# Performance work log

Measured on AMD Instinct MI355X. Metric: run time of the kernel, lower is better.

Reference implementation:

```python
import jax, jax.numpy as jnp
import numpy as np

INPUT_DIM = 256
EMBED_DIM = 256
NUM_HEADS = 8
HEAD_DIM = EMBED_DIM // NUM_HEADS
N_TOKENS = 11136
N_BATCH = 16


def _xavier(key, shape):
    fan_out, fan_in = shape
    bound = np.sqrt(6.0 / (fan_in + fan_out)).astype(np.float32)
    return jax.random.uniform(key, shape, jnp.float32, -bound, bound)


def setup_inputs() -> dict:
    key = jax.random.key(0)
    k_x, k_ids, k_qkv, k_o = jax.random.split(key, 4)
    x = jax.random.normal(k_x, (N_TOKENS, INPUT_DIM), jnp.float32)
    batch_ids = jnp.sort(jax.random.randint(k_ids, (N_TOKENS,), 0, N_BATCH)).astype(jnp.int32)
    qkv_w = _xavier(k_qkv, (3 * EMBED_DIM, INPUT_DIM))
    qkv_b = jnp.zeros((3 * EMBED_DIM,), jnp.float32)
    o_w = _xavier(k_o, (EMBED_DIM, EMBED_DIM))
    o_b = jnp.zeros((EMBED_DIM,), jnp.float32)
    return {"x": x, "batch_ids": batch_ids, "qkv_w": qkv_w, "qkv_b": qkv_b,
            "o_w": o_w, "o_b": o_b}


def reference(x, batch_ids, qkv_w, qkv_b, o_w, o_b):
    # batch_ids is concrete metadata (mirrors np.unique on CPU in the original).
    ids = np.asarray(batch_ids)
    vals, counts = np.unique(ids, return_counts=True)
    B = len(vals)
    S = int(counts.max())
    offsets = np.concatenate([np.zeros(1, np.int64), np.cumsum(counts)[:-1]])
    seg = np.searchsorted(vals, ids)               # segment index per token
    pos = np.arange(ids.shape[0]) - offsets[seg]   # position within segment

    qkv = x @ qkv_w.T + qkv_b                      # [N, 3E]
    # pad_sequence with padding_value=1 -> scatter tokens into an all-ones buffer
    fin = jnp.ones((B, S, 3 * EMBED_DIM), qkv.dtype).at[seg, pos].set(qkv)
    # padded rows sum to exactly 3E (all ones) -> mask True marks padding
    pad_mask = fin.sum(-1) >= fin.shape[-1]        # [B, S]

    qkv4 = fin.reshape(B, S, NUM_HEADS, 3 * HEAD_DIM).transpose(0, 2, 1, 3)
    q, k, v = jnp.split(qkv4, 3, axis=-1)          # each [B, H, S, hd]

    logits = jnp.einsum('bhqd,bhkd->bhqk', q, k) * (HEAD_DIM ** -0.5)
    logits = jnp.where(pad_mask[:, None, None, :], -jnp.inf, logits)
    attn = jax.nn.softmax(logits, axis=-1)         # [B, H, S, S]

    out = jnp.einsum('bhqk,bhkd->bhqd', attn, v)
    out = out.transpose(0, 2, 1, 3).reshape(B, S, EMBED_DIM)
    out = out[seg, pos]                            # unpad -> [N, E]
    return out @ o_w.T + o_b
```

## Files before the change

kernel.cpp:

```cpp
#include <hip/hip_runtime.h>
#include <stdint.h>


#define N_TOK 11136
#define E 256
#define H 8
#define HD 32

typedef __attribute__((ext_vector_type(8))) __bf16 bf16x8;
typedef __attribute__((ext_vector_type(8))) unsigned short u16x8;
typedef __attribute__((ext_vector_type(4))) float f32x4;

__device__ __forceinline__ unsigned short f2bf(float f) {
  unsigned int u = __float_as_uint(f);
  u = (u + 0x7FFFu + ((u >> 16) & 1u)) >> 16;
  return (unsigned short)u;
}
__device__ __forceinline__ float bf2f(unsigned short s) {
  return __uint_as_float(((unsigned int)s) << 16);
}
__device__ __forceinline__ bf16x8 ld8(const unsigned short* p) {
  return *(const bf16x8*)p;
}

__global__ void k_split(const float* __restrict__ x, const float* __restrict__ qw,
                        const float* __restrict__ ow, const int* __restrict__ ids,
                        unsigned short* __restrict__ xhi, unsigned short* __restrict__ xlo,
                        unsigned short* __restrict__ whi, unsigned short* __restrict__ wlo,
                        unsigned short* __restrict__ owb, int* __restrict__ offs) {
  if (blockIdx.x == 0 && threadIdx.x < 17) {
    int b = threadIdx.x, lo = 0, hi = N_TOK;
    while (lo < hi) { int mid = (lo + hi) >> 1; if (ids[mid] < b) lo = mid + 1; else hi = mid; }
    offs[b] = lo;
  }
  const int NX4 = N_TOK * E / 4;
  const int NW4 = 3 * E * E / 4;
  const int NO4 = E * E / 4;
  int total = NX4 + NW4 + NO4;
  for (int i = blockIdx.x * blockDim.x + threadIdx.x; i < total;
       i += gridDim.x * blockDim.x) {
    if (i < NX4) {
      float4 v = ((const float4*)x)[i];
      ushort4 hv, lv;
      hv.x = f2bf(v.x); lv.x = f2bf(v.x - bf2f(hv.x));
      hv.y = f2bf(v.y); lv.y = f2bf(v.y - bf2f(hv.y));
      hv.z = f2bf(v.z); lv.z = f2bf(v.z - bf2f(hv.z));
      hv.w = f2bf(v.w); lv.w = f2bf(v.w - bf2f(hv.w));
      ((ushort4*)xhi)[i] = hv; ((ushort4*)xlo)[i] = lv;
    } else if (i < NX4 + NW4) {
      int j = i - NX4;
      float4 v = ((const float4*)qw)[j];
      ushort4 hv, lv;
      hv.x = f2bf(v.x); lv.x = f2bf(v.x - bf2f(hv.x));
      hv.y = f2bf(v.y); lv.y = f2bf(v.y - bf2f(hv.y));
      hv.z = f2bf(v.z); lv.z = f2bf(v.z - bf2f(hv.z));
      hv.w = f2bf(v.w); lv.w = f2bf(v.w - bf2f(hv.w));
      ((ushort4*)whi)[j] = hv; ((ushort4*)wlo)[j] = lv;
    } else {
      int j = i - NX4 - NW4;
      float4 v = ((const float4*)ow)[j];
      ushort4 hv;
      hv.x = f2bf(v.x); hv.y = f2bf(v.y); hv.z = f2bf(v.z); hv.w = f2bf(v.w);
      ((ushort4*)owb)[j] = hv;
    }
  }
}

#define QK_BSTRIDE 264
#define QSCALE (0.17677669529663687f * 1.4426950408889634f)
__global__ __launch_bounds__(256, 3) void k_qkv(
    const unsigned short* __restrict__ xhi, const unsigned short* __restrict__ xlo,
    const unsigned short* __restrict__ whi, const unsigned short* __restrict__ wlo,
    const float* __restrict__ qkv_b,
    unsigned short* __restrict__ Qb, unsigned short* __restrict__ Kb,
    unsigned short* __restrict__ Vt) {
  int bid = blockIdx.x + 16 * blockIdx.y;
  int xcd = bid & 7;
  int j8 = bid >> 3;
  int colb = j8 & 15;
  int tile = (j8 >> 4) * 8 + xcd;
  if (tile >= 58) return;
  int col0 = colb * 48;
  __shared__ __align__(16) unsigned short Bhi[48 * QK_BSTRIDE];
  __shared__ __align__(16) unsigned short Blo[48 * QK_BSTRIDE];
  int tid = threadIdx.x;
  int w = tid >> 6, lane = tid & 63, m = lane & 15, quad = lane >> 4;
  int rowb = tile * 192 + w * 48;

  {
    const u16x8* wh8 = (const u16x8*)(whi + (size_t)col0 * E);
    const u16x8* wl8 = (const u16x8*)(wlo + (size_t)col0 * E);
#pragma unroll
    for (int i = 0; i < 6; ++i) {
      int flat = i * 256 + tid;
      int row = flat >> 5, c8 = flat & 31;
      *(u16x8*)(Bhi + row * QK_BSTRIDE + c8 * 8) = wh8[flat];
      *(u16x8*)(Blo + row * QK_BSTRIDE + c8 * 8) = wl8[flat];
    }
  }
  __syncthreads();

  f32x4 acc[3][3] = {};
  bf16x8 ahn[3], aln[3];
#pragma unroll
  for (int mt = 0; mt < 3; ++mt) {
    const size_t ro = (size_t)(rowb + mt * 16 + m) * E + quad * 8;
    ahn[mt] = ld8(xhi + ro);
    aln[mt] = ld8(xlo + ro);
  }
  for (int kc = 0; kc < 8; ++kc) {
    bf16x8 ah[3], al[3];
#pragma unroll
    for (int mt = 0; mt < 3; ++mt) { ah[mt] = ahn[mt]; al[mt] = aln[mt]; }
    int kon = (kc < 7 ? kc + 1 : kc) * 32 + quad * 8;
#pragma unroll
    for (int mt = 0; mt < 3; ++mt) {
      const size_t ro = (size_t)(rowb + mt * 16 + m) * E + kon;
      ahn[mt] = ld8(xhi + ro);
      aln[mt] = ld8(xlo + ro);
    }
    int ko = kc * 32 + quad * 8;
#pragma unroll
    for (int t = 0; t < 3; ++t) {
      bf16x8 bh = ld8(Bhi + (16 * t + m) * QK_BSTRIDE + ko);
      bf16x8 bl = ld8(Blo + (16 * t + m) * QK_BSTRIDE + ko);
#pragma unroll
      for (int mt = 0; mt < 3; ++mt) {
        acc[mt][t] = __builtin_amdgcn_mfma_f32_16x16x32_bf16(ah[mt], bh, acc[mt][t], 0, 0, 0);
        acc[mt][t] = __builtin_amdgcn_mfma_f32_16x16x32_bf16(ah[mt], bl, acc[mt][t], 0, 0, 0);
        acc[mt][t] = __builtin_amdgcn_mfma_f32_16x16x32_bf16(al[mt], bh, acc[mt][t], 0, 0, 0);
      }
    }
  }
#pragma unroll
  for (int t = 0; t < 3; ++t) {
    int j = col0 + 16 * t + m;
    int hd = j / 96;
    int rr = j - hd * 96;
    float bias = qkv_b[j];
#pragma unroll
    for (int mt = 0; mt < 3; ++mt) {
      int tokb = rowb + mt * 16 + quad * 4;
      if (rr < 64) {
        float qsc = (rr < 32) ? QSCALE : 1.0f;
        unsigned short* dst = (rr < 32) ? (Qb + (size_t)hd * N_TOK * HD + rr)
                                        : (Kb + (size_t)hd * N_TOK * HD + (rr - 32));
#pragma unroll
        for (int r = 0; r < 4; ++r)
          dst[(size_t)(tokb + r) * HD] = f2bf((acc[mt][t][r] + bias) * qsc);
      } else {
        int d = rr - 64;
        ushort4 pk;
        pk.x = f2bf(acc[mt][t][0] + bias); pk.y = f2bf(acc[mt][t][1] + bias);
        pk.z = f2bf(acc[mt][t][2] + bias); pk.w = f2bf(acc[mt][t][3] + bias);
        *(ushort4*)(Vt + (size_t)(hd * HD + d) * N_TOK + tokb) = pk;
      }
    }
  }
}

#define PSTRIDE 72
#define VSTR 72
__global__ __launch_bounds__(256, 4) void k_attn(
    const int* __restrict__ ids, const int* __restrict__ offs,
    const unsigned short* __restrict__ Qb, const unsigned short* __restrict__ Kb,
    const unsigned short* __restrict__ Vt,
    unsigned short* __restrict__ attnb) {
  __shared__ __align__(16) unsigned short Kl[2][64 * 32];
  __shared__ __align__(16) unsigned short Vl[2][32 * VSTR];
  __shared__ __align__(16) unsigned short ldsP[4][16 * PSTRIDE];
  __shared__ int bred[8];
  int tid = threadIdx.x;
  int w = tid >> 6, lane = tid & 63;
  int m = lane & 15, quad = lane >> 4;
  int h = blockIdx.x;
  int tok0 = blockIdx.y * 64;
  int q0 = tok0 + w * 16;
  unsigned short* P = ldsP[w];
  int tok = q0 + m;
  int b = ids[tok];
  int st = offs[b], en = offs[b + 1];
  int kmin = st, kmax = en, stM = st, enm = en;
#pragma unroll
  for (int d = 1; d <= 8; d <<= 1) {
    kmin = min(kmin, __shfl_xor(kmin, d));
    kmax = max(kmax, __shfl_xor(kmax, d));
    stM  = max(stM,  __shfl_xor(stM,  d));
    enm  = min(enm,  __shfl_xor(enm,  d));
  }
  if (lane == 0) { bred[w] = kmin; bred[4 + w] = kmax; }
  __syncthreads();
  int kminB = min(min(bred[0], bred[1]), min(bred[2], bred[3]));
  int kmaxB = max(max(bred[4], bred[5]), max(bred[6], bred[7]));
  int k0beg = kminB & ~63;

  const unsigned short* Kbase = Kb + (size_t)h * N_TOK * HD;
  const unsigned short* Vbase = Vt + (size_t)h * HD * N_TOK;
  bf16x8 qf = ld8(Qb + (size_t)(h * N_TOK + tok) * HD + quad * 8);

  int krow = w * 16 + (lane >> 2);
  int kgof = (lane & 3) * 8;
  int vrow = w * 8 + (lane >> 3);
  int vgof = (lane & 7) * 8;

  bf16x8 kg = ld8(Kbase + (size_t)(k0beg + krow) * HD + kgof);
  bf16x8 vg = ld8(Vbase + (size_t)vrow * N_TOK + k0beg + vgof);
  *(bf16x8*)(&Kl[0][krow * 32 + kgof]) = kg;
  *(bf16x8*)(&Vl[0][vrow * VSTR + vgof]) = vg;
  __syncthreads();

  float lsum = 0.f;
  f32x4 o0 = {}, o1 = {};
  int buf = 0;
  for (int k0 = k0beg; k0 < kmaxB; k0 += 64) {
    int k1 = (k0 + 64 < kmaxB) ? (k0 + 64) : k0;
    kg = ld8(Kbase + (size_t)(k1 + krow) * HD + kgof);
    vg = ld8(Vbase + (size_t)vrow * N_TOK + k1 + vgof);
    const unsigned short* Kc = &Kl[buf][0];
    const unsigned short* Vc = &Vl[buf][0];
    f32x4 s[4];
#pragma unroll
    for (int i = 0; i < 4; ++i) {
      bf16x8 kf = ld8(Kc + (16 * i + m) * 32 + quad * 8);
      f32x4 z = {};
      s[i] = __builtin_amdgcn_mfma_f32_16x16x32_bf16(kf, qf, z, 0, 0, 0);
    }
    bool interior = (k0 >= stM && k0 + 64 <= enm);
    int jb = k0 + quad * 4;
#pragma unroll
    for (int i = 0; i < 4; ++i) {
      float p[4];
#pragma unroll
      for (int r = 0; r < 4; ++r) {
        float sv = s[i][r];
        if (!interior) {
          int j = jb + 16 * i + r;
          sv = (j >= st && j < en) ? sv : -3e38f;
        }
        float e;
        asm("v_exp_f32 %0, %1" : "=v"(e) : "v"(sv));
        p[r] = e;
      }
      lsum += (p[0] + p[1]) + (p[2] + p[3]);
      unsigned int b0 = __float_as_uint(p[0]) + 0x8000u;
      unsigned int b1 = __float_as_uint(p[1]) + 0x8000u;
      unsigned int b2 = __float_as_uint(p[2]) + 0x8000u;
      unsigned int b3 = __float_as_uint(p[3]) + 0x8000u;
      uint2 pk;
      pk.x = (b1 & 0xFFFF0000u) | (b0 >> 16);
      pk.y = (b3 & 0xFFFF0000u) | (b2 >> 16);
      *(uint2*)(P + m * PSTRIDE + 16 * i + quad * 4) = pk;
    }
#pragma unroll
    for (int c = 0; c < 2; ++c) {
      bf16x8 pf  = ld8(P + m * PSTRIDE + 32 * c + quad * 8);
      bf16x8 vf0 = ld8(Vc + m * VSTR + 32 * c + quad * 8);
      bf16x8 vf1 = ld8(Vc + (16 + m) * VSTR + 32 * c + quad * 8);
      o0 = __builtin_amdgcn_mfma_f32_16x16x32_bf16(vf0, pf, o0, 0, 0, 0);
      o1 = __builtin_amdgcn_mfma_f32_16x16x32_bf16(vf1, pf, o1, 0, 0, 0);
    }
    *(bf16x8*)(&Kl[buf ^ 1][krow * 32 + kgof]) = kg;
    *(bf16x8*)(&Vl[buf ^ 1][vrow * VSTR + vgof]) = vg;
    __syncthreads();
    buf ^= 1;
  }
  lsum += __shfl_xor(lsum, 16);
  lsum += __shfl_xor(lsum, 32);
  float inv = 1.0f / lsum;
  ushort4 pk0, pk1;
  pk0.x = f2bf(o0[0] * inv); pk0.y = f2bf(o0[1] * inv);
  pk0.z = f2bf(o0[2] * inv); pk0.w = f2bf(o0[3] * inv);
  pk1.x = f2bf(o1[0] * inv); pk1.y = f2bf(o1[1] * inv);
  pk1.z = f2bf(o1[2] * inv); pk1.w = f2bf(o1[3] * inv);
  *(ushort4*)(attnb + (size_t)tok * E + h * HD + quad * 4) = pk0;
  *(ushort4*)(attnb + (size_t)tok * E + h * HD + 16 + quad * 4) = pk1;
}

__global__ __launch_bounds__(256, 4) void k_oproj(
    const unsigned short* __restrict__ attnb, const unsigned short* __restrict__ owb,
    const float* __restrict__ ob, float* __restrict__ out) {
  __shared__ __align__(16) unsigned short Bo[64 * QK_BSTRIDE];
  int tid = threadIdx.x;
  int w = tid >> 6, lane = tid & 63, m = lane & 15, quad = lane >> 4;
  int tok0 = blockIdx.x * 64, col0 = blockIdx.y * 64;
  {
    const u16x8* o8 = (const u16x8*)(owb + (size_t)col0 * E);
#pragma unroll
    for (int i = 0; i < 8; ++i) {
      int flat = i * 256 + tid;
      int row = flat >> 5, c8 = flat & 31;
      *(u16x8*)(Bo + row * QK_BSTRIDE + c8 * 8) = o8[flat];
    }
  }
  __syncthreads();
  f32x4 acc[4] = {};
  int arow = tok0 + 16 * w + m;
  const unsigned short* abase = attnb + (size_t)arow * E + quad * 8;
  bf16x8 an = ld8(abase);
  for (int kc = 0; kc < 8; ++kc) {
    bf16x8 a = an;
    an = ld8(abase + (kc < 7 ? kc + 1 : kc) * 32);
    int ko = kc * 32 + quad * 8;
#pragma unroll
    for (int t = 0; t < 4; ++t) {
      bf16x8 b = ld8(Bo + (16 * t + m) * QK_BSTRIDE + ko);
      acc[t] = __builtin_amdgcn_mfma_f32_16x16x32_bf16(a, b, acc[t], 0, 0, 0);
    }
  }
#pragma unroll
  for (int t = 0; t < 4; ++t) {
    int j = col0 + 16 * t + m;
    float bias = ob[j];
#pragma unroll
    for (int r = 0; r < 4; ++r) {
      int tok = tok0 + 16 * w + quad * 4 + r;
      out[(size_t)tok * E + j] = acc[t][r] + bias;
    }
  }
}

extern "C" void kernel_launch(void* const* d_in, const int* in_sizes, int n_in,
                              void* d_out, int out_size, void* d_ws, size_t ws_size,
                              hipStream_t stream) {
  const float* x   = (const float*)d_in[0];
  const int*   ids = (const int*)d_in[1];
  const float* qw  = (const float*)d_in[2];
  const float* qb  = (const float*)d_in[3];
  const float* ow  = (const float*)d_in[4];
  const float* ob  = (const float*)d_in[5];
  float* out = (float*)d_out;

  char* p = (char*)d_ws;
  auto alloc = [&](size_t bytes) {
    char* r = p;
    p += (bytes + 255) & ~(size_t)255;
    return r;
  };
  int* offs = (int*)alloc(32 * sizeof(int));
  unsigned short* xhi = (unsigned short*)alloc((size_t)N_TOK * E * 2);
  unsigned short* xlo = (unsigned short*)alloc((size_t)N_TOK * E * 2);
  unsigned short* whi = (unsigned short*)alloc((size_t)3 * E * E * 2);
  unsigned short* wlo = (unsigned short*)alloc((size_t)3 * E * E * 2);
  unsigned short* owb = (unsigned short*)alloc((size_t)E * E * 2);
  unsigned short* Qb  = (unsigned short*)alloc((size_t)N_TOK * E * 2);
  unsigned short* Kb  = (unsigned short*)alloc((size_t)N_TOK * E * 2);
  unsigned short* Vt  = (unsigned short*)alloc((size_t)N_TOK * E * 2);
  unsigned short* att = (unsigned short*)alloc((size_t)N_TOK * E * 2);

  k_split<<<dim3(1712), dim3(256), 0, stream>>>(x, qw, ow, ids, xhi, xlo, whi, wlo, owb, offs);
  k_qkv<<<dim3(16, 64), dim3(256), 0, stream>>>(xhi, xlo, whi, wlo, qb, Qb, Kb, Vt);
  k_attn<<<dim3(H, N_TOK / 64), dim3(256), 0, stream>>>(ids, offs, Qb, Kb, Vt, att);
  k_oproj<<<dim3(N_TOK / 64, E / 64), dim3(256), 0, stream>>>(att, owb, ob, out);
}
```

Measured before the change: 154.7 us.

## Process two query tiles per warp in attention to reuse K/V tiles

Each attention block now handles 128 query tokens instead of 64, with every wave computing two 16-row query tiles against the same K/V tile held in LDS. This halves the K/V global loads and LDS staging per query and doubles MFMA work per barrier, aiming to cut memory and synchronisation overhead. In exchange, register pressure and LDS use grow, the grid halves (8x87 blocks), and the key range per block widens, which may add masked work when a block straddles segment boundaries.

Measured after the change: 164.6 us. +6.4%, slower.

```diff
diff --git a/kernel.cpp b/kernel.cpp
--- a/kernel.cpp
+++ b/kernel.cpp
@@ -168,27 +168,29 @@
     unsigned short* __restrict__ attnb) {
   __shared__ __align__(16) unsigned short Kl[2][64 * 32];
   __shared__ __align__(16) unsigned short Vl[2][32 * VSTR];
-  __shared__ __align__(16) unsigned short ldsP[4][16 * PSTRIDE];
+  __shared__ __align__(16) unsigned short ldsP[8][16 * PSTRIDE];
   __shared__ int bred[8];
   int tid = threadIdx.x;
   int w = tid >> 6, lane = tid & 63;
   int m = lane & 15, quad = lane >> 4;
   int h = blockIdx.x;
-  int tok0 = blockIdx.y * 64;
-  int q0 = tok0 + w * 16;
-  unsigned short* P = ldsP[w];
-  int tok = q0 + m;
-  int b = ids[tok];
-  int st = offs[b], en = offs[b + 1];
-  int kmin = st, kmax = en, stM = st, enm = en;
+  int q0 = blockIdx.y * 128 + w * 16;
+  int tok0 = q0 + m, tok1 = q0 + 64 + m;
+  int b0 = ids[tok0], b1 = ids[tok1];
+  int st0 = offs[b0], en0 = offs[b0 + 1];
+  int st1 = offs[b1], en1 = offs[b1 + 1];
+  int kminW = min(st0, st1), kmaxW = max(en0, en1);
+  int stM0 = st0, enm0 = en0, stM1 = st1, enm1 = en1;
 #pragma unroll
   for (int d = 1; d <= 8; d <<= 1) {
-    kmin = min(kmin, __shfl_xor(kmin, d));
-    kmax = max(kmax, __shfl_xor(kmax, d));
-    stM  = max(stM,  __shfl_xor(stM,  d));
-    enm  = min(enm,  __shfl_xor(enm,  d));
-  }
-  if (lane == 0) { bred[w] = kmin; bred[4 + w] = kmax; }
+    kminW = min(kminW, __shfl_xor(kminW, d));
+    kmaxW = max(kmaxW, __shfl_xor(kmaxW, d));
+    stM0 = max(stM0, __shfl_xor(stM0, d));
+    enm0 = min(enm0, __shfl_xor(enm0, d));
+    stM1 = max(stM1, __shfl_xor(stM1, d));
+    enm1 = min(enm1, __shfl_xor(enm1, d));
+  }
+  if (lane == 0) { bred[w] = kminW; bred[4 + w] = kmaxW; }
   __syncthreads();
   int kminB = min(min(bred[0], bred[1]), min(bred[2], bred[3]));
   int kmaxB = max(max(bred[4], bred[5]), max(bred[6], bred[7]));
@@ -196,7 +198,10 @@
 
   const unsigned short* Kbase = Kb + (size_t)h * N_TOK * HD;
   const unsigned short* Vbase = Vt + (size_t)h * HD * N_TOK;
-  bf16x8 qf = ld8(Qb + (size_t)(h * N_TOK + tok) * HD + quad * 8);
+  bf16x8 qf0 = ld8(Qb + (size_t)(h * N_TOK + tok0) * HD + quad * 8);
+  bf16x8 qf1 = ld8(Qb + (size_t)(h * N_TOK + tok1) * HD + quad * 8);
+  unsigned short* P0 = ldsP[2 * w];
+  unsigned short* P1 = ldsP[2 * w + 1];
 
   int krow = w * 16 + (lane >> 2);
   int kgof = (lane & 3) * 8;
@@ -209,8 +214,8 @@
   *(bf16x8*)(&Vl[0][vrow * VSTR + vgof]) = vg;
   __syncthreads();
 
-  float lsum = 0.f;
-  f32x4 o0 = {}, o1 = {};
+  float lsum0 = 0.f, lsum1 = 0.f;
+  f32x4 o00 = {}, o01 = {}, o10 = {}, o11 = {};
   int buf = 0;
   for (int k0 = k0beg; k0 < kmaxB; k0 += 64) {
     int k1 = (k0 + 64 < kmaxB) ? (k0 + 64) : k0;
@@ -218,62 +223,101 @@
     vg = ld8(Vbase + (size_t)vrow * N_TOK + k1 + vgof);
     const unsigned short* Kc = &Kl[buf][0];
     const unsigned short* Vc = &Vl[buf][0];
-    f32x4 s[4];
+    f32x4 s0[4], s1[4];
 #pragma unroll
     for (int i = 0; i < 4; ++i) {
       bf16x8 kf = ld8(Kc + (16 * i + m) * 32 + quad * 8);
       f32x4 z = {};
-      s[i] = __builtin_amdgcn_mfma_f32_16x16x32_bf16(kf, qf, z, 0, 0, 0);
-    }
-    bool interior = (k0 >= stM && k0 + 64 <= enm);
+      s0[i] = __builtin_amdgcn_mfma_f32_16x16x32_bf16(kf, qf0, z, 0, 0, 0);
+      s1[i] = __builtin_amdgcn_mfma_f32_16x16x32_bf16(kf, qf1, z, 0, 0, 0);
+    }
     int jb = k0 + quad * 4;
-#pragma unroll
-    for (int i = 0; i < 4; ++i) {
-      float p[4];
-#pragma unroll
-      for (int r = 0; r < 4; ++r) {
-        float sv = s[i][r];
-        if (!interior) {
-          int j = jb + 16 * i + r;
-          sv = (j >= st && j < en) ? sv : -3e38f;
+    {
+      bool interior = (k0 >= stM0 && k0 + 64 <= enm0);
+#pragma unroll
+      for (int i = 0; i < 4; ++i) {
+        float p[4];
+#pragma unroll
+        for (int r = 0; r < 4; ++r) {
+          float sv = s0[i][r];
+          if (!interior) {
+            int j = jb + 16 * i + r;
+            sv = (j >= st0 && j < en0) ? sv : -3e38f;
+          }
+          float e;
+          asm("v_exp_f32 %0, %1" : "=v"(e) : "v"(sv));
+          p[r] = e;
         }
-        float e;
-        asm("v_exp_f32 %0, %1" : "=v"(e) : "v"(sv));
-        p[r] = e;
+        lsum0 += (p[0] + p[1]) + (p[2] + p[3]);
+        unsigned int c0 = __float_as_uint(p[0]) + 0x8000u;
+        unsigned int c1 = __float_as_uint(p[1]) + 0x8000u;
+        unsigned int c2 = __float_as_uint(p[2]) + 0x8000u;
+        unsigned int c3 = __float_as_uint(p[3]) + 0x8000u;
+        uint2 pk;
+        pk.x = (c1 & 0xFFFF0000u) | (c0 >> 16);
+        pk.y = (c3 & 0xFFFF0000u) | (c2 >> 16);
+        *(uint2*)(P0 + m * PSTRIDE + 16 * i + quad * 4) = pk;
       }
-      lsum += (p[0] + p[1]) + (p[2] + p[3]);
-      unsigned int b0 = __float_as_uint(p[0]) + 0x8000u;
-      unsigned int b1 = __float_as_uint(p[1]) + 0x8000u;
-      unsigned int b2 = __float_as_uint(p[2]) + 0x8000u;
-      unsigned int b3 = __float_as_uint(p[3]) + 0x8000u;
-      uint2 pk;
-      pk.x = (b1 & 0xFFFF0000u) | (b0 >> 16);
-      pk.y = (b3 & 0xFFFF0000u) | (b2 >> 16);
-      *(uint2*)(P + m * PSTRIDE + 16 * i + quad * 4) = pk;
+    }
+    {
+      bool interior = (k0 >= stM1 && k0 + 64 <= enm1);
+#pragma unroll
+      for (int i = 0; i < 4; ++i) {
+        float p[4];
+#pragma unroll
+        for (int r = 0; r < 4; ++r) {
+          float sv = s1[i][r];
+          if (!interior) {
+            int j = jb + 16 * i + r;
+            sv = (j >= st1 && j < en1) ? sv : -3e38f;
+          }
+          float e;
+          asm("v_exp_f32 %0, %1" : "=v"(e) : "v"(sv));
+          p[r] = e;
+        }
+        lsum1 += (p[0] + p[1]) + (p[2] + p[3]);
+        unsigned int c0 = __float_as_uint(p[0]) + 0x8000u;
+        unsigned int c1 = __float_as_uint(p[1]) + 0x8000u;
+        unsigned int c2 = __float_as_uint(p[2]) + 0x8000u;
+        unsigned int c3 = __float_as_uint(p[3]) + 0x8000u;
+        uint2 pk;
+        pk.x = (c1 & 0xFFFF0000u) | (c0 >> 16);
+        pk.y = (c3 & 0xFFFF0000u) | (c2 >> 16);
+        *(uint2*)(P1 + m * PSTRIDE + 16 * i + quad * 4) = pk;
+      }
     }
 #pragma unroll
     for (int c = 0; c < 2; ++c) {
-      bf16x8 pf  = ld8(P + m * PSTRIDE + 32 * c + quad * 8);
       bf16x8 vf0 = ld8(Vc + m * VSTR + 32 * c + quad * 8);
       bf16x8 vf1 = ld8(Vc + (16 + m) * VSTR + 32 * c + quad * 8);
-      o0 = __builtin_amdgcn_mfma_f32_16x16x32_bf16(vf0, pf, o0, 0, 0, 0);
-      o1 = __builtin_amdgcn_mfma_f32_16x16x32_bf16(vf1, pf, o1, 0, 0, 0);
+      bf16x8 pf0 = ld8(P0 + m * PSTRIDE + 32 * c + quad * 8);
+      bf16x8 pf1 = ld8(P1 + m * PSTRIDE + 32 * c + quad * 8);
+      o00 = __builtin_amdgcn_mfma_f32_16x16x32_bf16(vf0, pf0, o00, 0, 0, 0);
+      o01 = __builtin_amdgcn_mfma_f32_16x16x32_bf16(vf1, pf0, o01, 0, 0, 0);
+      o10 = __builtin_amdgcn_mfma_f32_16x16x32_bf16(vf0, pf1, o10, 0, 0, 0);
+      o11 = __builtin_amdgcn_mfma_f32_16x16x32_bf16(vf1, pf1, o11, 0, 0, 0);
     }
     *(bf16x8*)(&Kl[buf ^ 1][krow * 32 + kgof]) = kg;
     *(bf16x8*)(&Vl[buf ^ 1][vrow * VSTR + vgof]) = vg;
     __syncthreads();
     buf ^= 1;
   }
-  lsum += __shfl_xor(lsum, 16);
-  lsum += __shfl_xor(lsum, 32);
-  float inv = 1.0f / lsum;
+  lsum0 += __shfl_xor(lsum0, 16); lsum0 += __shfl_xor(lsum0, 32);
+  lsum1 += __shfl_xor(lsum1, 16); lsum1 += __shfl_xor(lsum1, 32);
+  float inv0 = 1.0f / lsum0, inv1 = 1.0f / lsum1;
   ushort4 pk0, pk1;
-  pk0.x = f2bf(o0[0] * inv); pk0.y = f2bf(o0[1] * inv);
-  pk0.z = f2bf(o0[2] * inv); pk0.w = f2bf(o0[3] * inv);
-  pk1.x = f2bf(o1[0] * inv); pk1.y = f2bf(o1[1] * inv);
-  pk1.z = f2bf(o1[2] * inv); pk1.w = f2bf(o1[3] * inv);
-  *(ushort4*)(attnb + (size_t)tok * E + h * HD + quad * 4) = pk0;
-  *(ushort4*)(attnb + (size_t)tok * E + h * HD + 16 + quad * 4) = pk1;
+  pk0.x = f2bf(o00[0] * inv0); pk0.y = f2bf(o00[1] * inv0);
+  pk0.z = f2bf(o00[2] * inv0); pk0.w = f2bf(o00[3] * inv0);
+  pk1.x = f2bf(o01[0] * inv0); pk1.y = f2bf(o01[1] * inv0);
+  pk1.z = f2bf(o01[2] * inv0); pk1.w = f2bf(o01[3] * inv0);
+  *(ushort4*)(attnb + (size_t)tok0 * E + h * HD + quad * 4) = pk0;
+  *(ushort4*)(attnb + (size_t)tok0 * E + h * HD + 16 + quad * 4) = pk1;
+  pk0.x = f2bf(o10[0] * inv1); pk0.y = f2bf(o10[1] * inv1);
+  pk0.z = f2bf(o10[2] * inv1); pk0.w = f2bf(o10[3] * inv1);
+  pk1.x = f2bf(o11[0] * inv1); pk1.y = f2bf(o11[1] * inv1);
+  pk1.z = f2bf(o11[2] * inv1); pk1.w = f2bf(o11[3] * inv1);
+  *(ushort4*)(attnb + (size_t)tok1 * E + h * HD + quad * 4) = pk0;
+  *(ushort4*)(attnb + (size_t)tok1 * E + h * HD + 16 + quad * 4) = pk1;
 }
 
 __global__ __launch_bounds__(256, 4) void k_oproj(
@@ -349,6 +393,6 @@
 
   k_split<<<dim3(1712), dim3(256), 0, stream>>>(x, qw, ow, ids, xhi, xlo, whi, wlo, owb, offs);
   k_qkv<<<dim3(16, 64), dim3(256), 0, stream>>>(xhi, xlo, whi, wlo, qb, Qb, Kb, Vt);
-  k_attn<<<dim3(H, N_TOK / 64), dim3(256), 0, stream>>>(ids, offs, Qb, Kb, Vt, att);
+  k_attn<<<dim3(H, N_TOK / 128), dim3(256), 0, stream>>>(ids, offs, Qb, Kb, Vt, att);
   k_oproj<<<dim3(N_TOK / 64, E / 64), dim3(256), 0, stream>>>(att, owb, ob, out);
 }
```

## Split attention key range in two and merge partials in output projection

Applied to the files above, without the earlier changes.

The attention kernel's grid gains a z dimension of 2. Each block handles half of the key chunks for its query tile and writes unnormalized fp32 partial outputs plus row sums. The output-projection kernel then adds the two partials, divides by the combined sum and converts to bf16 before the MFMA. This doubles attention parallelism and halves each block's serial loop. In exchange it writes and reads much larger fp32 intermediates, and each k_oproj block re-reads both partials for every column tile. The merge relies on the softmax using no running max, so partial sums can simply be added.

New measurement: 163.9 us. +5.9%, slower.

```diff
diff --git a/kernel.cpp b/kernel.cpp
--- a/kernel.cpp
+++ b/kernel.cpp
@@ -165,7 +165,7 @@
     const int* __restrict__ ids, const int* __restrict__ offs,
     const unsigned short* __restrict__ Qb, const unsigned short* __restrict__ Kb,
     const unsigned short* __restrict__ Vt,
-    unsigned short* __restrict__ attnb) {
+    float* __restrict__ Opart, float* __restrict__ Ls) {
   __shared__ __align__(16) unsigned short Kl[2][64 * 32];
   __shared__ __align__(16) unsigned short Vl[2][32 * VSTR];
   __shared__ __align__(16) unsigned short ldsP[4][16 * PSTRIDE];
@@ -174,8 +174,8 @@
   int w = tid >> 6, lane = tid & 63;
   int m = lane & 15, quad = lane >> 4;
   int h = blockIdx.x;
-  int tok0 = blockIdx.y * 64;
-  int q0 = tok0 + w * 16;
+  int ks = blockIdx.z;
+  int q0 = blockIdx.y * 64 + w * 16;
   unsigned short* P = ldsP[w];
   int tok = q0 + m;
   int b = ids[tok];
@@ -193,6 +193,10 @@
   int kminB = min(min(bred[0], bred[1]), min(bred[2], bred[3]));
   int kmaxB = max(max(bred[4], bred[5]), max(bred[6], bred[7]));
   int k0beg = kminB & ~63;
+  int nch = (kmaxB - k0beg + 63) >> 6;
+  int half = (nch + 1) >> 1;
+  int cs = ks ? half : 0;
+  int ce = ks ? nch : half;
 
   const unsigned short* Kbase = Kb + (size_t)h * N_TOK * HD;
   const unsigned short* Vbase = Vt + (size_t)h * HD * N_TOK;
@@ -203,8 +207,9 @@
   int vrow = w * 8 + (lane >> 3);
   int vgof = (lane & 7) * 8;
 
-  bf16x8 kg = ld8(Kbase + (size_t)(k0beg + krow) * HD + kgof);
-  bf16x8 vg = ld8(Vbase + (size_t)vrow * N_TOK + k0beg + vgof);
+  int kpro = k0beg + min(cs, nch - 1) * 64;
+  bf16x8 kg = ld8(Kbase + (size_t)(kpro + krow) * HD + kgof);
+  bf16x8 vg = ld8(Vbase + (size_t)vrow * N_TOK + kpro + vgof);
   *(bf16x8*)(&Kl[0][krow * 32 + kgof]) = kg;
   *(bf16x8*)(&Vl[0][vrow * VSTR + vgof]) = vg;
   __syncthreads();
@@ -212,8 +217,9 @@
   float lsum = 0.f;
   f32x4 o0 = {}, o1 = {};
   int buf = 0;
-  for (int k0 = k0beg; k0 < kmaxB; k0 += 64) {
-    int k1 = (k0 + 64 < kmaxB) ? (k0 + 64) : k0;
+  for (int ci = cs; ci < ce; ++ci) {
+    int k0 = k0beg + ci * 64;
+    int k1 = (ci + 1 < ce) ? (k0 + 64) : k0;
     kg = ld8(Kbase + (size_t)(k1 + krow) * HD + kgof);
     vg = ld8(Vbase + (size_t)vrow * N_TOK + k1 + vgof);
     const unsigned short* Kc = &Kl[buf][0];
@@ -266,18 +272,15 @@
   }
   lsum += __shfl_xor(lsum, 16);
   lsum += __shfl_xor(lsum, 32);
-  float inv = 1.0f / lsum;
-  ushort4 pk0, pk1;
-  pk0.x = f2bf(o0[0] * inv); pk0.y = f2bf(o0[1] * inv);
-  pk0.z = f2bf(o0[2] * inv); pk0.w = f2bf(o0[3] * inv);
-  pk1.x = f2bf(o1[0] * inv); pk1.y = f2bf(o1[1] * inv);
-  pk1.z = f2bf(o1[2] * inv); pk1.w = f2bf(o1[3] * inv);
-  *(ushort4*)(attnb + (size_t)tok * E + h * HD + quad * 4) = pk0;
-  *(ushort4*)(attnb + (size_t)tok * E + h * HD + 16 + quad * 4) = pk1;
+  float* Op = Opart + (size_t)ks * N_TOK * E;
+  *(f32x4*)(Op + (size_t)tok * E + h * HD + quad * 4) = o0;
+  *(f32x4*)(Op + (size_t)tok * E + h * HD + 16 + quad * 4) = o1;
+  if (quad == 0) Ls[(size_t)(ks * H + h) * N_TOK + tok] = lsum;
 }
 
 __global__ __launch_bounds__(256, 4) void k_oproj(
-    const unsigned short* __restrict__ attnb, const unsigned short* __restrict__ owb,
+    const float* __restrict__ Opart, const float* __restrict__ Ls,
+    const unsigned short* __restrict__ owb,
     const float* __restrict__ ob, float* __restrict__ out) {
   __shared__ __align__(16) unsigned short Bo[64 * QK_BSTRIDE];
   int tid = threadIdx.x;
@@ -293,18 +296,36 @@
     }
   }
   __syncthreads();
+  int arow = tok0 + 16 * w + m;
+  float invl[8];
+#pragma unroll
+  for (int hh = 0; hh < 8; ++hh) {
+    float l0 = Ls[(size_t)hh * N_TOK + arow];
+    float l1 = Ls[(size_t)(8 + hh) * N_TOK + arow];
+    invl[hh] = 1.0f / (l0 + l1);
+  }
+  const float* a0 = Opart + (size_t)arow * E + quad * 8;
+  const float* a1 = Opart + (size_t)N_TOK * E + (size_t)arow * E + quad * 8;
   f32x4 acc[4] = {};
-  int arow = tok0 + 16 * w + m;
-  const unsigned short* abase = attnb + (size_t)arow * E + quad * 8;
-  bf16x8 an = ld8(abase);
+  float4 nu0 = *(const float4*)(a0), nu1 = *(const float4*)(a0 + 4);
+  float4 nv0 = *(const float4*)(a1), nv1 = *(const float4*)(a1 + 4);
   for (int kc = 0; kc < 8; ++kc) {
-    bf16x8 a = an;
-    an = ld8(abase + (kc < 7 ? kc + 1 : kc) * 32);
+    float4 u0 = nu0, u1 = nu1, v0 = nv0, v1 = nv1;
+    int kn = (kc < 7 ? kc + 1 : kc) * 32;
+    nu0 = *(const float4*)(a0 + kn); nu1 = *(const float4*)(a0 + kn + 4);
+    nv0 = *(const float4*)(a1 + kn); nv1 = *(const float4*)(a1 + kn + 4);
+    float iv = invl[kc];
+    u16x8 ar;
+    ar[0] = f2bf((u0.x + v0.x) * iv); ar[1] = f2bf((u0.y + v0.y) * iv);
+    ar[2] = f2bf((u0.z + v0.z) * iv); ar[3] = f2bf((u0.w + v0.w) * iv);
+    ar[4] = f2bf((u1.x + v1.x) * iv); ar[5] = f2bf((u1.y + v1.y) * iv);
+    ar[6] = f2bf((u1.z + v1.z) * iv); ar[7] = f2bf((u1.w + v1.w) * iv);
+    bf16x8 a = __builtin_bit_cast(bf16x8, ar);
     int ko = kc * 32 + quad * 8;
 #pragma unroll
     for (int t = 0; t < 4; ++t) {
-      bf16x8 b = ld8(Bo + (16 * t + m) * QK_BSTRIDE + ko);
-      acc[t] = __builtin_amdgcn_mfma_f32_16x16x32_bf16(a, b, acc[t], 0, 0, 0);
+      bf16x8 bfr = ld8(Bo + (16 * t + m) * QK_BSTRIDE + ko);
+      acc[t] = __builtin_amdgcn_mfma_f32_16x16x32_bf16(a, bfr, acc[t], 0, 0, 0);
     }
   }
 #pragma unroll
@@ -345,10 +366,11 @@
   unsigned short* Qb  = (unsigned short*)alloc((size_t)N_TOK * E * 2);
   unsigned short* Kb  = (unsigned short*)alloc((size_t)N_TOK * E * 2);
   unsigned short* Vt  = (unsigned short*)alloc((size_t)N_TOK * E * 2);
-  unsigned short* att = (unsigned short*)alloc((size_t)N_TOK * E * 2);
+  float* Opart = (float*)alloc((size_t)2 * N_TOK * E * 4);
+  float* Ls    = (float*)alloc((size_t)2 * H * N_TOK * 4);
 
   k_split<<<dim3(1712), dim3(256), 0, stream>>>(x, qw, ow, ids, xhi, xlo, whi, wlo, owb, offs);
   k_qkv<<<dim3(16, 64), dim3(256), 0, stream>>>(xhi, xlo, whi, wlo, qb, Qb, Kb, Vt);
-  k_attn<<<dim3(H, N_TOK / 64), dim3(256), 0, stream>>>(ids, offs, Qb, Kb, Vt, att);
-  k_oproj<<<dim3(N_TOK / 64, E / 64), dim3(256), 0, stream>>>(att, owb, ob, out);
-}
+  k_attn<<<dim3(H, N_TOK / 64, 2), dim3(256), 0, stream>>>(ids, offs, Qb, Kb, Vt, Opart, Ls);
+  k_oproj<<<dim3(N_TOK / 64, E / 64), dim3(256), 0, stream>>>(Opart, Ls, owb, ob, out);
+}
```
